# Kernel optimization log

Hardware: AMD Instinct MI355X
Metric: run time of the kernel (lower is better)

## Reference

```python
import jax, jax.numpy as jnp
import numpy as np

V = 32000   # vocab / input_size
H = 1024    # hidden_size (== embedding dim)
L = 2       # num_layers
B = 64      # batch
T = 256     # seq_len


def setup_inputs() -> dict:
    key = jax.random.key(0)
    ks = jax.random.split(key, 8)
    s = float(1.0 / np.sqrt(H))  # pytorch default uniform bound for LSTM/Linear
    return {
        "inputs": jax.random.randint(ks[0], (B, T), 0, V),
        "embed_table": jax.random.normal(ks[1], (V, H), jnp.float32),
        "W_ih": jax.random.uniform(ks[2], (L, 4 * H, H), jnp.float32, -s, s),
        "W_hh": jax.random.uniform(ks[3], (L, 4 * H, H), jnp.float32, -s, s),
        "b_ih": jax.random.uniform(ks[4], (L, 4 * H), jnp.float32, -s, s),
        "b_hh": jax.random.uniform(ks[5], (L, 4 * H), jnp.float32, -s, s),
        "W_proj": jax.random.uniform(ks[6], (V, H), jnp.float32, -s, s),
        "b_proj": jnp.zeros((V,), jnp.float32),  # module fills bias with 0
    }


def _lstm_layer(x, Wih, Whh, bih, bhh):
    # x: [B, T, H]. Precompute input contribution for all steps (one big GEMM).
    xg = jnp.einsum("bth,gh->btg", x, Wih) + bih + bhh  # [B, T, 4H]
    h0 = jnp.zeros((x.shape[0], Whh.shape[1]), x.dtype)
    c0 = h0

    def step(carry, xt):
        h, c = carry
        gates = xt + h @ Whh.T  # [B, 4H]
        i, f, g, o = jnp.split(gates, 4, axis=-1)  # pytorch gate order i,f,g,o
        i = jax.nn.sigmoid(i)
        f = jax.nn.sigmoid(f)
        g = jnp.tanh(g)
        o = jax.nn.sigmoid(o)
        c = f * c + i * g
        h = o * jnp.tanh(c)
        return (h, c), h

    (hT, cT), ys = jax.lax.scan(step, (h0, c0), jnp.swapaxes(xg, 0, 1))
    return jnp.swapaxes(ys, 0, 1), hT, cT  # [B,T,H], [B,H], [B,H]


def reference(inputs, embed_table, W_ih, W_hh, b_ih, b_hh, W_proj, b_proj):
    x = embed_table[inputs]  # [B, T, H]
    h_n, c_n = [], []
    for l in range(L):  # small fixed layer loop
        x, hT, cT = _lstm_layer(x, W_ih[l], W_hh[l], b_ih[l], b_hh[l])
        h_n.append(hT)
        c_n.append(cT)
    last_output = x[:, -1]                      # squeeze(output[:, -1]) with B>1 -> [B, H]
    logits = last_output @ W_proj.T + b_proj    # [B, V]
    return last_output, logits, jnp.stack(h_n), jnp.stack(c_n)
```

## Files before the change

kernel.cpp:

```cpp
#include <hip/hip_runtime.h>
#include <hip/hip_bf16.h>
#include <stdint.h>
#include <stddef.h>

typedef __hip_bfloat16 bf16;
typedef __attribute__((ext_vector_type(8))) short bfrag;
typedef __attribute__((ext_vector_type(4))) float ffrag;

#define HDIM 1024
#define BATCH 64
#define TSTEPS 256
#define GDIM 4096
#define VOCAB 32000

#define HSLOT 16384ull

__device__ __forceinline__ float b2f(bf16 x) { return __bfloat162float(x); }
__device__ __forceinline__ bf16 f2b(float x) { return __float2bfloat16(x); }
__device__ __forceinline__ short f2bs(float x) {
  bf16 b = __float2bfloat16(x);
  return *reinterpret_cast<short*>(&b);
}
__device__ __forceinline__ float bs2f(unsigned short u) {
  union { unsigned int i; float f; } v;
  v.i = ((unsigned int)u) << 16;
  return v.f;
}
__device__ __forceinline__ ffrag mfma16(bfrag a, bfrag b, ffrag c) {
  return __builtin_amdgcn_mfma_f32_16x16x32_bf16(a, b, c, 0, 0, 0);
}
__device__ __forceinline__ float sigm(float x) { return 1.0f / (1.0f + __expf(-x)); }
__device__ __forceinline__ float tanhfast(float x) {
  float e = __expf(2.0f * x);
  return 1.0f - 2.0f / (e + 1.0f);
}

__device__ __forceinline__ void store_u16_agent(unsigned short* p, unsigned short v) {
  __hip_atomic_store(p, v, __ATOMIC_RELAXED, __HIP_MEMORY_SCOPE_AGENT);
}
__device__ __forceinline__ unsigned long long load_u64_agent(const unsigned long long* p) {
  return __hip_atomic_load(p, __ATOMIC_RELAXED, __HIP_MEMORY_SCOPE_AGENT);
}
__device__ __forceinline__ void store_u32_agent(unsigned* p, unsigned v) {
  __hip_atomic_store(p, v, __ATOMIC_RELAXED, __HIP_MEMORY_SCOPE_AGENT);
}

__global__ void convert_bf16_kernel(const float* __restrict__ src, bf16* __restrict__ dst, int n4) {
  int i = blockIdx.x * 256 + threadIdx.x;
  if (i >= n4) return;
  float4 v = reinterpret_cast<const float4*>(src)[i];
  ushort4 o;
  o.x = (unsigned short)f2bs(v.x);
  o.y = (unsigned short)f2bs(v.y);
  o.z = (unsigned short)f2bs(v.z);
  o.w = (unsigned short)f2bs(v.w);
  reinterpret_cast<ushort4*>(dst)[i] = o;
}

__global__ void embed_kernel(const int* __restrict__ ids, const float* __restrict__ table,
                             bf16* __restrict__ x, int n4) {
  int i = blockIdx.x * 256 + threadIdx.x;
  if (i >= n4) return;
  int row = i >> 8;
  int c4 = i & 255;
  int tok = ids[row];
  float4 v = reinterpret_cast<const float4*>(table)[(size_t)tok * 256 + c4];
  ushort4 o;
  o.x = (unsigned short)f2bs(v.x);
  o.y = (unsigned short)f2bs(v.y);
  o.z = (unsigned short)f2bs(v.z);
  o.w = (unsigned short)f2bs(v.w);
  reinterpret_cast<ushort4*>(x)[i] = o;
}

#define BMX 128
#define BNX 128
#define BKX 64

template<int LYR>
__launch_bounds__(256, 2)
__global__ void gemm_xg_kernel(const bf16* __restrict__ A,
                               const bf16* __restrict__ W,
                               const float* __restrict__ bih,
                               const float* __restrict__ bhh,
                               bf16* __restrict__ xg) {
  __shared__ bf16 As[BMX][BKX + 8];
  __shared__ bf16 Bs[BNX][BKX + 8];
  const int n0 = blockIdx.x * BNX;
  const int m0 = blockIdx.y * BMX;
  const int tid = threadIdx.x;
  const int w = tid >> 6, l = tid & 63;
  const int wm = (w >> 1) * 64, wn = (w & 1) * 64;
  const int lr = l & 15, lk = (l >> 4) * 8;

  ffrag acc[4][4];
#pragma unroll
  for (int i = 0; i < 4; ++i)
#pragma unroll
    for (int j = 0; j < 4; ++j) acc[i][j] = ffrag{0.f, 0.f, 0.f, 0.f};

  const int sr = tid >> 1, sh = (tid & 1) * 32;
  for (int kb = 0; kb < HDIM; kb += BKX) {
    __syncthreads();
    {
      if (LYR == 0) {
        const uint4* ga = reinterpret_cast<const uint4*>(&A[(size_t)(m0 + sr) * HDIM + kb + sh]);
        uint4* la = reinterpret_cast<uint4*>(&As[sr][sh]);
        la[0] = ga[0]; la[1] = ga[1]; la[2] = ga[2]; la[3] = ga[3];
      } else {
        const unsigned long long* hb = (const unsigned long long*)A;
        const int m = m0 + sr;
        const size_t tb = (size_t)(255 - (m >> 6)) * HSLOT + (m & 63);
        const int kg0 = (kb + sh) >> 3;
#pragma unroll
        for (int ii = 0; ii < 4; ++ii) {
          unsigned long long lo = hb[tb + (size_t)(kg0 + ii) * 64];
          unsigned long long hi = hb[tb + 8192 + (size_t)(kg0 + ii) * 64];
          *(unsigned long long*)&As[sr][sh + ii * 8]     = lo;
          *(unsigned long long*)&As[sr][sh + ii * 8 + 4] = hi;
        }
      }
      const uint4* gb = reinterpret_cast<const uint4*>(&W[(size_t)(n0 + sr) * HDIM + kb + sh]);
      uint4* lb = reinterpret_cast<uint4*>(&Bs[sr][sh]);
      lb[0] = gb[0]; lb[1] = gb[1]; lb[2] = gb[2]; lb[3] = gb[3];
    }
    __syncthreads();
#pragma unroll
    for (int ks = 0; ks < 2; ++ks) {
      const int ko = ks * 32 + lk;
      bfrag af[4], bfv[4];
#pragma unroll
      for (int i = 0; i < 4; ++i)
        af[i] = *reinterpret_cast<const bfrag*>(&As[wm + i * 16 + lr][ko]);
#pragma unroll
      for (int j = 0; j < 4; ++j)
        bfv[j] = *reinterpret_cast<const bfrag*>(&Bs[wn + j * 16 + lr][ko]);
#pragma unroll
      for (int i = 0; i < 4; ++i)
#pragma unroll
        for (int j = 0; j < 4; ++j)
          acc[i][j] = mfma16(af[i], bfv[j], acc[i][j]);
    }
  }
  const int rg = (l >> 4) * 4;
#pragma unroll
  for (int j = 0; j < 4; ++j) {
    const int n = n0 + wn + j * 16 + lr;
    const float bias = bih[n] + bhh[n];
    const int q = n >> 10, g = (n & 1023) >> 3, jj = n & 7;
    bf16* base = xg + (size_t)(q * 128 + g) * 16384 * 8 + jj;
#pragma unroll
    for (int i = 0; i < 4; ++i) {
#pragma unroll
      for (int r = 0; r < 4; ++r) {
        const int m = m0 + wm + i * 16 + rg + r;
        base[(size_t)m * 8] = f2b(acc[i][j][r] + bias);
      }
    }
  }
}

__launch_bounds__(128, 1)
__global__ void lstm_seq_kernel(const bf16* __restrict__ xg,
                                const bf16* __restrict__ Whh,
                                bf16* hist,
                                float* __restrict__ out_h,
                                float* __restrict__ out_c,
                                float* __restrict__ out_last,
                                unsigned* __restrict__ flags,
                                int xbs, int xts) {
  __shared__ float gxp[2][16][33];
  const int wgid = blockIdx.x;
  const int bg = wgid & 3, cg = wgid >> 2;
  const int tid = threadIdx.x;
  const int w = tid >> 6, l = tid & 63;
  const int lr = l & 15, lkg = l >> 4;
  const int kh = w, kbase = kh * 512;

  bfrag breg0[16], breg1[16];
  {
    const int q = lr >> 2, ja = lr & 3;
    const size_t g0 = ((size_t)q * HDIM + cg * 8 + ja) * HDIM + kbase + lkg * 8;
    const size_t g1 = ((size_t)q * HDIM + cg * 8 + 4 + ja) * HDIM + kbase + lkg * 8;
#pragma unroll
    for (int ks = 0; ks < 16; ++ks) {
      breg0[ks] = *reinterpret_cast<const bfrag*>(&Whh[g0 + ks * 32]);
      breg1[ks] = *reinterpret_cast<const bfrag*>(&Whh[g1 + ks * 32]);
    }
  }

  const int eb = tid & 15;
  const int ejj = tid >> 4;
  const int b_glob = bg * 16 + eb;
  const int j_glob = cg * 8 + ejj;
  const int set = ejj >> 2, jn = ejj & 3;
  float c = 0.0f;

  unsigned long long* hb = (unsigned long long*)hist;
  const size_t hbase = (size_t)(kh * 64 + lkg) * 64 + bg * 16 + lr;

  const bf16* xq0 = xg + (size_t)(0 * 128 + cg) * 16384 * 8 + ejj;
  const bf16* xq1 = xg + (size_t)(1 * 128 + cg) * 16384 * 8 + ejj;
  const bf16* xq2 = xg + (size_t)(2 * 128 + cg) * 16384 * 8 + ejj;
  const bf16* xq3 = xg + (size_t)(3 * 128 + cg) * 16384 * 8 + ejj;
  unsigned short xv0, xv1, xv2, xv3;
  {
    const size_t xidx = (size_t)b_glob * xbs;
    xv0 = *(const unsigned short*)&xq0[xidx * 8];
    xv1 = *(const unsigned short*)&xq1[xidx * 8];
    xv2 = *(const unsigned short*)&xq2[xidx * 8];
    xv3 = *(const unsigned short*)&xq3[xidx * 8];
  }

  const unsigned long long* fv = (const unsigned long long*)flags + (size_t)bg * 128;

#pragma unroll 1
  for (int t = 0; t < TSTEPS; ++t) {
    if (t > 0) {
      const unsigned tt = (unsigned)t;
      for (;;) {
        unsigned long long fa = load_u64_agent(&fv[l]);
        unsigned long long fb = load_u64_agent(&fv[64 + l]);
        int ok = ((unsigned)fa >= tt) && ((unsigned)(fa >> 32) >= tt) &&
                 ((unsigned)fb >= tt) && ((unsigned)(fb >> 32) >= tt);
        if (__all(ok)) break;
        __builtin_amdgcn_s_sleep(1);
      }
    }
    __builtin_amdgcn_sched_barrier(0);
    asm volatile("" ::: "memory");

    const unsigned long long* hin = hb + (size_t)(TSTEPS - t) * HSLOT;
    ffrag a0 = ffrag{0.f, 0.f, 0.f, 0.f};
    ffrag a1 = ffrag{0.f, 0.f, 0.f, 0.f};
#pragma unroll
    for (int ks = 0; ks < 16; ++ks) {
      union { unsigned long long u[2]; bfrag f; } au;
      au.u[0] = hin[hbase + ks * 256];
      au.u[1] = hin[8192 + hbase + ks * 256];
      a0 = mfma16(au.f, breg0[ks], a0);
      a1 = mfma16(au.f, breg1[ks], a1);
    }
#pragma unroll
    for (int r = 0; r < 4; ++r) {
      gxp[kh][lkg * 4 + r][lr]      = a0[r];
      gxp[kh][lkg * 4 + r][16 + lr] = a1[r];
    }
    __syncthreads();

    const float gi = gxp[0][eb][set * 16 + jn]      + gxp[1][eb][set * 16 + jn]      + bs2f(xv0);
    const float gf = gxp[0][eb][set * 16 + 4 + jn]  + gxp[1][eb][set * 16 + 4 + jn]  + bs2f(xv1);
    const float gg = gxp[0][eb][set * 16 + 8 + jn]  + gxp[1][eb][set * 16 + 8 + jn]  + bs2f(xv2);
    const float go = gxp[0][eb][set * 16 + 12 + jn] + gxp[1][eb][set * 16 + 12 + jn] + bs2f(xv3);
    const float iv = sigm(gi), fvv = sigm(gf), gv = tanhfast(gg), ov = sigm(go);
    c = fvv * c + iv * gv;
    const float h = ov * tanhfast(c);
    const unsigned short hbits = (unsigned short)f2bs(h);

    unsigned long long* hout = hb + (size_t)(255 - t) * HSLOT;
    unsigned short* hp = (unsigned short*)(hout + (size_t)set * 8192 + cg * 64 + b_glob) + jn;
    store_u16_agent(hp, hbits);

    if (t < TSTEPS - 1) {
      __builtin_amdgcn_s_waitcnt(0);
      if (l == 0) store_u32_agent(&flags[bg * 256 + cg * 2 + w], (unsigned)(t + 1));
      const size_t xidx = (size_t)b_glob * xbs + (size_t)(t + 1) * xts;
      xv0 = *(const unsigned short*)&xq0[xidx * 8];
      xv1 = *(const unsigned short*)&xq1[xidx * 8];
      xv2 = *(const unsigned short*)&xq2[xidx * 8];
      xv3 = *(const unsigned short*)&xq3[xidx * 8];
    } else {
      out_h[(size_t)b_glob * HDIM + j_glob] = h;
      out_c[(size_t)b_glob * HDIM + j_glob] = c;
      if (out_last) out_last[(size_t)b_glob * HDIM + j_glob] = h;
    }
  }
}

__launch_bounds__(256, 2)
__global__ void logits_kernel(const bf16* __restrict__ hfin,
                              const float* __restrict__ Wp,
                              const float* __restrict__ bp,
                              float* __restrict__ out) {
  const int tid = threadIdx.x;
  const int w = tid >> 6, l = tid & 63;
  const int lr = l & 15, lkg = l >> 4, lk = lkg * 8;
  const int col = blockIdx.x * 64 + w * 16 + lr;
  const float* wrow = &Wp[(size_t)col * HDIM];
  const unsigned long long* hb = (const unsigned long long*)hfin;
  ffrag acc[4];
#pragma unroll
  for (int i = 0; i < 4; ++i) acc[i] = ffrag{0.f, 0.f, 0.f, 0.f};
#pragma unroll 2
  for (int ks = 0; ks < 32; ++ks) {
    const int k = ks * 32 + lk;
    float4 wa = *reinterpret_cast<const float4*>(&wrow[k]);
    float4 wb = *reinterpret_cast<const float4*>(&wrow[k + 4]);
    bfrag bv;
    bv[0] = f2bs(wa.x); bv[1] = f2bs(wa.y); bv[2] = f2bs(wa.z); bv[3] = f2bs(wa.w);
    bv[4] = f2bs(wb.x); bv[5] = f2bs(wb.y); bv[6] = f2bs(wb.z); bv[7] = f2bs(wb.w);
    const size_t kg = (size_t)(ks * 4 + lkg);
#pragma unroll
    for (int i = 0; i < 4; ++i) {
      union { unsigned long long u[2]; bfrag f; } av;
      av.u[0] = hb[kg * 64 + i * 16 + lr];
      av.u[1] = hb[8192 + kg * 64 + i * 16 + lr];
      acc[i] = mfma16(av.f, bv, acc[i]);
    }
  }
  const float bias = bp[col];
#pragma unroll
  for (int i = 0; i < 4; ++i) {
#pragma unroll
    for (int r = 0; r < 4; ++r) {
      const int b = i * 16 + (l >> 4) * 4 + r;
      out[(size_t)b * VOCAB + col] = acc[i][r] + bias;
    }
  }
}

extern "C" void kernel_launch(void* const* d_in, const int* in_sizes, int n_in,
                              void* d_out, int out_size, void* d_ws, size_t ws_size,
                              hipStream_t stream) {
  const int*   ids   = (const int*)d_in[0];
  const float* table = (const float*)d_in[1];
  const float* Wih   = (const float*)d_in[2];
  const float* Whh   = (const float*)d_in[3];
  const float* bih   = (const float*)d_in[4];
  const float* bhh   = (const float*)d_in[5];
  const float* Wp    = (const float*)d_in[6];
  const float* bp    = (const float*)d_in[7];
  float* out = (float*)d_out;

  char* ws = (char*)d_ws;
  const size_t HISTB = 257ull * 131072ull;
  const size_t OFF_XG  = 0;
  const size_t OFF_HA  = OFF_XG + (size_t)512 * 16384 * 8 * 2;
  const size_t OFF_HB  = OFF_HA + HISTB;
  const size_t OFF_WIH = OFF_HB + HISTB;
  const size_t OFF_WHH = OFF_WIH + (size_t)2 * GDIM * HDIM * 2;
  const size_t OFF_SYNC= OFF_WHH + (size_t)2 * GDIM * HDIM * 2;

  bf16* xg    = (bf16*)(ws + OFF_XG);
  bf16* xb    = (bf16*)(ws + OFF_HA);
  bf16* histA = (bf16*)(ws + OFF_HA);
  bf16* histB = (bf16*)(ws + OFF_HB);
  bf16* wihb  = (bf16*)(ws + OFF_WIH);
  bf16* whhb  = (bf16*)(ws + OFF_WHH);
  unsigned* sync = (unsigned*)(ws + OFF_SYNC);

  (void)hipMemsetAsync(sync, 0, 16384, stream);
  (void)hipMemsetAsync(ws + OFF_HA + 33554432ull, 0, 131072, stream);
  (void)hipMemsetAsync(ws + OFF_HB + 33554432ull, 0, 131072, stream);

  const int nconv4 = 2 * GDIM * HDIM / 4;
  convert_bf16_kernel<<<nconv4 / 256, 256, 0, stream>>>(Wih, wihb, nconv4);
  convert_bf16_kernel<<<nconv4 / 256, 256, 0, stream>>>(Whh, whhb, nconv4);
  const int nemb4 = BATCH * TSTEPS * HDIM / 4;
  embed_kernel<<<nemb4 / 256, 256, 0, stream>>>(ids, table, xb, nemb4);

  float* out_last   = out;
  float* out_logits = out + 65536;
  float* out_hn     = out + 2113536;
  float* out_cn     = out + 2244608;

  gemm_xg_kernel<0><<<dim3(GDIM / BNX, (BATCH * TSTEPS) / BMX), 256, 0, stream>>>(
      xb, wihb, bih, bhh, xg);
  lstm_seq_kernel<<<512, 128, 0, stream>>>(
      xg, whhb, histA, out_hn, out_cn, nullptr, sync, 256, 1);

  gemm_xg_kernel<1><<<dim3(GDIM / BNX, (BATCH * TSTEPS) / BMX), 256, 0, stream>>>(
      histA, wihb + (size_t)GDIM * HDIM, bih + GDIM, bhh + GDIM, xg);
  lstm_seq_kernel<<<512, 128, 0, stream>>>(
      xg, whhb + (size_t)GDIM * HDIM, histB,
      out_hn + (size_t)BATCH * HDIM, out_cn + (size_t)BATCH * HDIM,
      out_last, sync + 1024, 1, 64);

  logits_kernel<<<VOCAB / 64, 256, 0, stream>>>(histB, Wp, bp, out_logits);
}
```

Before: 2.315 ms.

## Fuse both LSTM layers into one wavefront-pipelined persistent kernel

The separate layer-2 input GEMM and the two sequential recurrence kernels are replaced by one persistent kernel with 768 blocks. 256 blocks run the layer-1 recurrence, and 512 blocks run layer 2, computing the W_ih·y and W_hh·h contributions per step from register-resident weights. Layer 2 step s waits on layer-1 flags for step s, so the two layers overlap as a wavefront. This removes a full GEMM pass and one kernel's serial latency. The cost is more per-step MFMA work in the layer-2 blocks and a requirement that all 768 blocks be co-resident (3 per CU), or the spin-waits can deadlock.

```diff
diff --git a/kernel.cpp b/kernel.cpp
--- a/kernel.cpp
+++ b/kernel.cpp
@@ -6,6 +6,7 @@
 typedef __hip_bfloat16 bf16;
 typedef __attribute__((ext_vector_type(8))) short bfrag;
 typedef __attribute__((ext_vector_type(4))) float ffrag;
+typedef unsigned long long u64;
 
 #define HDIM 1024
 #define BATCH 64
@@ -15,7 +16,6 @@
 
 #define HSLOT 16384ull
 
-__device__ __forceinline__ float b2f(bf16 x) { return __bfloat162float(x); }
 __device__ __forceinline__ bf16 f2b(float x) { return __float2bfloat16(x); }
 __device__ __forceinline__ short f2bs(float x) {
   bf16 b = __float2bfloat16(x);
@@ -38,7 +38,7 @@
 __device__ __forceinline__ void store_u16_agent(unsigned short* p, unsigned short v) {
   __hip_atomic_store(p, v, __ATOMIC_RELAXED, __HIP_MEMORY_SCOPE_AGENT);
 }
-__device__ __forceinline__ unsigned long long load_u64_agent(const unsigned long long* p) {
+__device__ __forceinline__ u64 load_u64_agent(const u64* p) {
   return __hip_atomic_load(p, __ATOMIC_RELAXED, __HIP_MEMORY_SCOPE_AGENT);
 }
 __device__ __forceinline__ void store_u32_agent(unsigned* p, unsigned v) {
@@ -77,7 +77,6 @@
 #define BNX 128
 #define BKX 64
 
-template<int LYR>
 __launch_bounds__(256, 2)
 __global__ void gemm_xg_kernel(const bf16* __restrict__ A,
                                const bf16* __restrict__ W,
@@ -103,23 +102,9 @@
   for (int kb = 0; kb < HDIM; kb += BKX) {
     __syncthreads();
     {
-      if (LYR == 0) {
-        const uint4* ga = reinterpret_cast<const uint4*>(&A[(size_t)(m0 + sr) * HDIM + kb + sh]);
-        uint4* la = reinterpret_cast<uint4*>(&As[sr][sh]);
-        la[0] = ga[0]; la[1] = ga[1]; la[2] = ga[2]; la[3] = ga[3];
-      } else {
-        const unsigned long long* hb = (const unsigned long long*)A;
-        const int m = m0 + sr;
-        const size_t tb = (size_t)(255 - (m >> 6)) * HSLOT + (m & 63);
-        const int kg0 = (kb + sh) >> 3;
-#pragma unroll
-        for (int ii = 0; ii < 4; ++ii) {
-          unsigned long long lo = hb[tb + (size_t)(kg0 + ii) * 64];
-          unsigned long long hi = hb[tb + 8192 + (size_t)(kg0 + ii) * 64];
-          *(unsigned long long*)&As[sr][sh + ii * 8]     = lo;
-          *(unsigned long long*)&As[sr][sh + ii * 8 + 4] = hi;
-        }
-      }
+      const uint4* ga = reinterpret_cast<const uint4*>(&A[(size_t)(m0 + sr) * HDIM + kb + sh]);
+      uint4* la = reinterpret_cast<uint4*>(&As[sr][sh]);
+      la[0] = ga[0]; la[1] = ga[1]; la[2] = ga[2]; la[3] = ga[3];
       const uint4* gb = reinterpret_cast<const uint4*>(&W[(size_t)(n0 + sr) * HDIM + kb + sh]);
       uint4* lb = reinterpret_cast<uint4*>(&Bs[sr][sh]);
       lb[0] = gb[0]; lb[1] = gb[1]; lb[2] = gb[2]; lb[3] = gb[3];
@@ -160,119 +145,221 @@
   }
 }
 
-__launch_bounds__(128, 1)
-__global__ void lstm_seq_kernel(const bf16* __restrict__ xg,
-                                const bf16* __restrict__ Whh,
-                                bf16* hist,
-                                float* __restrict__ out_h,
-                                float* __restrict__ out_c,
-                                float* __restrict__ out_last,
-                                unsigned* __restrict__ flags,
-                                int xbs, int xts) {
-  __shared__ float gxp[2][16][33];
-  const int wgid = blockIdx.x;
-  const int bg = wgid & 3, cg = wgid >> 2;
+__launch_bounds__(256, 3)
+__global__ void fused2_kernel(const bf16* __restrict__ xg,
+                              const bf16* __restrict__ whh1,
+                              const bf16* __restrict__ whh2,
+                              const bf16* __restrict__ wih2,
+                              const float* __restrict__ bih2,
+                              const float* __restrict__ bhh2,
+                              bf16* histA, bf16* histB,
+                              float* __restrict__ out_h1, float* __restrict__ out_c1,
+                              float* __restrict__ out_h2, float* __restrict__ out_c2,
+                              float* __restrict__ out_last,
+                              unsigned* __restrict__ fL1,
+                              unsigned* __restrict__ fL2) {
+  __shared__ float gxp[2][16][65];
+  const int id = blockIdx.x;
   const int tid = threadIdx.x;
   const int w = tid >> 6, l = tid & 63;
   const int lr = l & 15, lkg = l >> 4;
-  const int kh = w, kbase = kh * 512;
-
-  bfrag breg0[16], breg1[16];
-  {
-    const int q = lr >> 2, ja = lr & 3;
-    const size_t g0 = ((size_t)q * HDIM + cg * 8 + ja) * HDIM + kbase + lkg * 8;
-    const size_t g1 = ((size_t)q * HDIM + cg * 8 + 4 + ja) * HDIM + kbase + lkg * 8;
-#pragma unroll
-    for (int ks = 0; ks < 16; ++ks) {
-      breg0[ks] = *reinterpret_cast<const bfrag*>(&Whh[g0 + ks * 32]);
-      breg1[ks] = *reinterpret_cast<const bfrag*>(&Whh[g1 + ks * 32]);
-    }
-  }
-
-  const int eb = tid & 15;
-  const int ejj = tid >> 4;
-  const int b_glob = bg * 16 + eb;
-  const int j_glob = cg * 8 + ejj;
-  const int set = ejj >> 2, jn = ejj & 3;
-  float c = 0.0f;
-
-  unsigned long long* hb = (unsigned long long*)hist;
-  const size_t hbase = (size_t)(kh * 64 + lkg) * 64 + bg * 16 + lr;
-
-  const bf16* xq0 = xg + (size_t)(0 * 128 + cg) * 16384 * 8 + ejj;
-  const bf16* xq1 = xg + (size_t)(1 * 128 + cg) * 16384 * 8 + ejj;
-  const bf16* xq2 = xg + (size_t)(2 * 128 + cg) * 16384 * 8 + ejj;
-  const bf16* xq3 = xg + (size_t)(3 * 128 + cg) * 16384 * 8 + ejj;
-  unsigned short xv0, xv1, xv2, xv3;
-  {
-    const size_t xidx = (size_t)b_glob * xbs;
-    xv0 = *(const unsigned short*)&xq0[xidx * 8];
-    xv1 = *(const unsigned short*)&xq1[xidx * 8];
-    xv2 = *(const unsigned short*)&xq2[xidx * 8];
-    xv3 = *(const unsigned short*)&xq3[xidx * 8];
-  }
-
-  const unsigned long long* fv = (const unsigned long long*)flags + (size_t)bg * 128;
+  const int kh = w >> 1;
+  const int q = lr >> 2, jn = lr & 3;
+
+  if (id < 256) {
+    const int bg = id & 3, cg16 = id >> 2;
+    const int ch = w & 1;
+    bfrag breg0[16], breg1[16];
+    {
+      const int colbase = cg16 * 16 + ch * 8;
+      const size_t r0 = ((size_t)q * HDIM + colbase + jn) * HDIM + kh * 512 + lkg * 8;
+      const size_t r1 = ((size_t)q * HDIM + colbase + 4 + jn) * HDIM + kh * 512 + lkg * 8;
+#pragma unroll
+      for (int ks = 0; ks < 16; ++ks) {
+        breg0[ks] = *reinterpret_cast<const bfrag*>(&whh1[r0 + ks * 32]);
+        breg1[ks] = *reinterpret_cast<const bfrag*>(&whh1[r1 + ks * 32]);
+      }
+    }
+    const int eb = tid & 15, cl = tid >> 4;
+    const int gpl = cg16 * 2 + (cl >> 3);
+    const int xjj = cl & 7;
+    const int kgs = cg16 * 2 + (cl >> 3);
+    const int shalf = (cl >> 2) & 1, sjj = cl & 3;
+    float c = 0.0f;
+
+    u64* hb = (u64*)histA;
+    const size_t arow = (size_t)(kh * 64 + lkg) * 64 + bg * 16 + lr;
+    const u64* fv = (const u64*)fL1 + (size_t)bg * 128;
+    const unsigned short* xgu = (const unsigned short*)xg;
+
+    unsigned short xn[4];
+#pragma unroll
+    for (int qq = 0; qq < 4; ++qq)
+      xn[qq] = xgu[(((size_t)qq * 128 + gpl) * 16384 + (size_t)(bg * 16 + eb) * 256) * 8 + xjj];
 
 #pragma unroll 1
-  for (int t = 0; t < TSTEPS; ++t) {
-    if (t > 0) {
-      const unsigned tt = (unsigned)t;
-      for (;;) {
-        unsigned long long fa = load_u64_agent(&fv[l]);
-        unsigned long long fb = load_u64_agent(&fv[64 + l]);
-        int ok = ((unsigned)fa >= tt) && ((unsigned)(fa >> 32) >= tt) &&
-                 ((unsigned)fb >= tt) && ((unsigned)(fb >> 32) >= tt);
-        if (__all(ok)) break;
-        __builtin_amdgcn_s_sleep(1);
-      }
-    }
-    __builtin_amdgcn_sched_barrier(0);
-    asm volatile("" ::: "memory");
-
-    const unsigned long long* hin = hb + (size_t)(TSTEPS - t) * HSLOT;
-    ffrag a0 = ffrag{0.f, 0.f, 0.f, 0.f};
-    ffrag a1 = ffrag{0.f, 0.f, 0.f, 0.f};
-#pragma unroll
-    for (int ks = 0; ks < 16; ++ks) {
-      union { unsigned long long u[2]; bfrag f; } au;
-      au.u[0] = hin[hbase + ks * 256];
-      au.u[1] = hin[8192 + hbase + ks * 256];
-      a0 = mfma16(au.f, breg0[ks], a0);
-      a1 = mfma16(au.f, breg1[ks], a1);
-    }
-#pragma unroll
-    for (int r = 0; r < 4; ++r) {
-      gxp[kh][lkg * 4 + r][lr]      = a0[r];
-      gxp[kh][lkg * 4 + r][16 + lr] = a1[r];
-    }
-    __syncthreads();
-
-    const float gi = gxp[0][eb][set * 16 + jn]      + gxp[1][eb][set * 16 + jn]      + bs2f(xv0);
-    const float gf = gxp[0][eb][set * 16 + 4 + jn]  + gxp[1][eb][set * 16 + 4 + jn]  + bs2f(xv1);
-    const float gg = gxp[0][eb][set * 16 + 8 + jn]  + gxp[1][eb][set * 16 + 8 + jn]  + bs2f(xv2);
-    const float go = gxp[0][eb][set * 16 + 12 + jn] + gxp[1][eb][set * 16 + 12 + jn] + bs2f(xv3);
-    const float iv = sigm(gi), fvv = sigm(gf), gv = tanhfast(gg), ov = sigm(go);
-    c = fvv * c + iv * gv;
-    const float h = ov * tanhfast(c);
-    const unsigned short hbits = (unsigned short)f2bs(h);
-
-    unsigned long long* hout = hb + (size_t)(255 - t) * HSLOT;
-    unsigned short* hp = (unsigned short*)(hout + (size_t)set * 8192 + cg * 64 + b_glob) + jn;
-    store_u16_agent(hp, hbits);
-
-    if (t < TSTEPS - 1) {
+    for (int t = 0; t < TSTEPS; ++t) {
+      if (t > 0) {
+        const unsigned tt = (unsigned)t;
+        for (;;) {
+          u64 fa = load_u64_agent(&fv[l]);
+          u64 fb = load_u64_agent(&fv[64 + l]);
+          int ok = ((unsigned)fa >= tt) && ((unsigned)(fa >> 32) >= tt) &&
+                   ((unsigned)fb >= tt) && ((unsigned)(fb >> 32) >= tt);
+          if (__all(ok)) break;
+          __builtin_amdgcn_s_sleep(1);
+        }
+      }
+      __builtin_amdgcn_sched_barrier(0);
+      asm volatile("" ::: "memory");
+
+      const u64* hin = hb + (size_t)(TSTEPS - t) * HSLOT;
+      ffrag a0 = ffrag{0.f, 0.f, 0.f, 0.f};
+      ffrag a1 = ffrag{0.f, 0.f, 0.f, 0.f};
+#pragma unroll
+      for (int ks = 0; ks < 16; ++ks) {
+        union { u64 u[2]; bfrag f; } au;
+        au.u[0] = hin[arow + ks * 256];
+        au.u[1] = hin[8192 + arow + ks * 256];
+        a0 = mfma16(au.f, breg0[ks], a0);
+        a1 = mfma16(au.f, breg1[ks], a1);
+      }
+      {
+        const int cb = (w & 1) * 8;
+#pragma unroll
+        for (int r = 0; r < 4; ++r) {
+          gxp[kh][lkg * 4 + r][q * 16 + cb + jn]     = a0[r];
+          gxp[kh][lkg * 4 + r][q * 16 + cb + 4 + jn] = a1[r];
+        }
+      }
+      __syncthreads();
+
+      const float gi = gxp[0][eb][cl]      + gxp[1][eb][cl]      + bs2f(xn[0]);
+      const float gf = gxp[0][eb][16 + cl] + gxp[1][eb][16 + cl] + bs2f(xn[1]);
+      const float gg = gxp[0][eb][32 + cl] + gxp[1][eb][32 + cl] + bs2f(xn[2]);
+      const float go = gxp[0][eb][48 + cl] + gxp[1][eb][48 + cl] + bs2f(xn[3]);
+      c = sigm(gf) * c + sigm(gi) * tanhfast(gg);
+      const float h = sigm(go) * tanhfast(c);
+
+      u64* hout = hb + (size_t)(255 - t) * HSLOT;
+      store_u16_agent((unsigned short*)(hout + (size_t)shalf * 8192 + kgs * 64 + bg * 16 + eb) + sjj,
+                      (unsigned short)f2bs(h));
+      if (t == TSTEPS - 1) {
+        const int col = cg16 * 16 + cl;
+        out_h1[(size_t)(bg * 16 + eb) * HDIM + col] = h;
+        out_c1[(size_t)(bg * 16 + eb) * HDIM + col] = c;
+      }
       __builtin_amdgcn_s_waitcnt(0);
-      if (l == 0) store_u32_agent(&flags[bg * 256 + cg * 2 + w], (unsigned)(t + 1));
-      const size_t xidx = (size_t)b_glob * xbs + (size_t)(t + 1) * xts;
-      xv0 = *(const unsigned short*)&xq0[xidx * 8];
-      xv1 = *(const unsigned short*)&xq1[xidx * 8];
-      xv2 = *(const unsigned short*)&xq2[xidx * 8];
-      xv3 = *(const unsigned short*)&xq3[xidx * 8];
-    } else {
-      out_h[(size_t)b_glob * HDIM + j_glob] = h;
-      out_c[(size_t)b_glob * HDIM + j_glob] = c;
-      if (out_last) out_last[(size_t)b_glob * HDIM + j_glob] = h;
+      if (l == 0) store_u32_agent(&fL1[bg * 256 + cg16 * 4 + w], (unsigned)(t + 1));
+      if (t < TSTEPS - 1) {
+#pragma unroll
+        for (int qq = 0; qq < 4; ++qq)
+          xn[qq] = xgu[(((size_t)qq * 128 + gpl) * 16384 +
+                        (size_t)(bg * 16 + eb) * 256 + t + 1) * 8 + xjj];
+      }
+      __syncthreads();
+      __builtin_amdgcn_sched_barrier(0);
+    }
+  } else {
+    const int sid = id - 256;
+    const int bg = sid & 3, cg8 = sid >> 2;
+    const int ch4 = w & 1;
+    bfrag wregH[16], wregY[16];
+    {
+      const int colbase = cg8 * 8 + ch4 * 4;
+      const size_t rr = ((size_t)q * HDIM + colbase + jn) * HDIM + kh * 512 + lkg * 8;
+#pragma unroll
+      for (int ks = 0; ks < 16; ++ks) {
+        wregH[ks] = *reinterpret_cast<const bfrag*>(&whh2[rr + ks * 32]);
+        wregY[ks] = *reinterpret_cast<const bfrag*>(&wih2[rr + ks * 32]);
+      }
+    }
+    const int eb = tid & 15, jc = tid >> 4;
+    float biasq[4];
+    if (tid < 128) {
+#pragma unroll
+      for (int qq = 0; qq < 4; ++qq) {
+        const int n = qq * HDIM + cg8 * 8 + jc;
+        biasq[qq] = bih2[n] + bhh2[n];
+      }
+    }
+    float c = 0.0f;
+
+    const u64* hbA = (const u64*)histA;
+    u64* hbB = (u64*)histB;
+    const size_t arow = (size_t)(kh * 64 + lkg) * 64 + bg * 16 + lr;
+    const u64* f1 = (const u64*)fL1 + (size_t)bg * 128;
+    const u64* f2d = (const u64*)fL2 + (size_t)bg * 64;
+
+#pragma unroll 1
+    for (int s = 0; s < TSTEPS; ++s) {
+      {
+        const unsigned tt = (unsigned)(s + 1);
+        for (;;) {
+          u64 fa = load_u64_agent(&f1[l]);
+          u64 fb = load_u64_agent(&f1[64 + l]);
+          int ok = ((unsigned)fa >= tt) && ((unsigned)(fa >> 32) >= tt) &&
+                   ((unsigned)fb >= tt) && ((unsigned)(fb >> 32) >= tt);
+          if (__all(ok)) break;
+          __builtin_amdgcn_s_sleep(2);
+        }
+      }
+      if (s > 0) {
+        const unsigned tt = (unsigned)s;
+        for (;;) {
+          u64 v = load_u64_agent(&f2d[l]);
+          int ok = ((unsigned)v >= tt) && ((unsigned)(v >> 32) >= tt);
+          if (__all(ok)) break;
+          __builtin_amdgcn_s_sleep(1);
+        }
+      }
+      __builtin_amdgcn_sched_barrier(0);
+      asm volatile("" ::: "memory");
+
+      const u64* yin = hbA + (size_t)(255 - s) * HSLOT;
+      const u64* hin = hbB + (size_t)(256 - s) * HSLOT;
+      ffrag acc = ffrag{0.f, 0.f, 0.f, 0.f};
+#pragma unroll
+      for (int ks = 0; ks < 16; ++ks) {
+        union { u64 u[2]; bfrag f; } au;
+        au.u[0] = yin[arow + ks * 256];
+        au.u[1] = yin[8192 + arow + ks * 256];
+        acc = mfma16(au.f, wregY[ks], acc);
+      }
+#pragma unroll
+      for (int ks = 0; ks < 16; ++ks) {
+        union { u64 u[2]; bfrag f; } au;
+        au.u[0] = hin[arow + ks * 256];
+        au.u[1] = hin[8192 + arow + ks * 256];
+        acc = mfma16(au.f, wregH[ks], acc);
+      }
+#pragma unroll
+      for (int r = 0; r < 4; ++r)
+        gxp[kh][lkg * 4 + r][q * 8 + ch4 * 4 + jn] = acc[r];
+      __syncthreads();
+
+      if (tid < 128) {
+        const float gi = gxp[0][eb][jc]      + gxp[1][eb][jc]      + biasq[0];
+        const float gf = gxp[0][eb][8 + jc]  + gxp[1][eb][8 + jc]  + biasq[1];
+        const float gg = gxp[0][eb][16 + jc] + gxp[1][eb][16 + jc] + biasq[2];
+        const float go = gxp[0][eb][24 + jc] + gxp[1][eb][24 + jc] + biasq[3];
+        c = sigm(gf) * c + sigm(gi) * tanhfast(gg);
+        const float h = sigm(go) * tanhfast(c);
+        u64* hout = hbB + (size_t)(255 - s) * HSLOT;
+        store_u16_agent((unsigned short*)(hout + (size_t)(jc >> 2) * 8192 + cg8 * 64 + bg * 16 + eb) +
+                            (jc & 3),
+                        (unsigned short)f2bs(h));
+        if (s == TSTEPS - 1) {
+          const int col = cg8 * 8 + jc;
+          out_h2[(size_t)(bg * 16 + eb) * HDIM + col] = h;
+          out_c2[(size_t)(bg * 16 + eb) * HDIM + col] = c;
+          out_last[(size_t)(bg * 16 + eb) * HDIM + col] = h;
+        }
+        __builtin_amdgcn_s_waitcnt(0);
+      }
+      __syncthreads();
+      if (tid == 0) store_u32_agent(&fL2[bg * 128 + cg8], (unsigned)(s + 1));
+      __builtin_amdgcn_sched_barrier(0);
     }
   }
 }
@@ -287,7 +374,7 @@
   const int lr = l & 15, lkg = l >> 4, lk = lkg * 8;
   const int col = blockIdx.x * 64 + w * 16 + lr;
   const float* wrow = &Wp[(size_t)col * HDIM];
-  const unsigned long long* hb = (const unsigned long long*)hfin;
+  const u64* hb = (const u64*)hfin;
   ffrag acc[4];
 #pragma unroll
   for (int i = 0; i < 4; ++i) acc[i] = ffrag{0.f, 0.f, 0.f, 0.f};
@@ -302,7 +389,7 @@
     const size_t kg = (size_t)(ks * 4 + lkg);
 #pragma unroll
     for (int i = 0; i < 4; ++i) {
-      union { unsigned long long u[2]; bfrag f; } av;
+      union { u64 u[2]; bfrag f; } av;
       av.u[0] = hb[kg * 64 + i * 16 + lr];
       av.u[1] = hb[8192 + kg * 64 + i * 16 + lr];
       acc[i] = mfma16(av.f, bv, acc[i]);
@@ -333,11 +420,11 @@
   float* out = (float*)d_out;
 
   char* ws = (char*)d_ws;
-  const size_t HISTB = 257ull * 131072ull;
+  const size_t HISTB_SZ = 257ull * 131072ull;
   const size_t OFF_XG  = 0;
   const size_t OFF_HA  = OFF_XG + (size_t)512 * 16384 * 8 * 2;
-  const size_t OFF_HB  = OFF_HA + HISTB;
-  const size_t OFF_WIH = OFF_HB + HISTB;
+  const size_t OFF_HB  = OFF_HA + HISTB_SZ;
+  const size_t OFF_WIH = OFF_HB + HISTB_SZ;
   const size_t OFF_WHH = OFF_WIH + (size_t)2 * GDIM * HDIM * 2;
   const size_t OFF_SYNC= OFF_WHH + (size_t)2 * GDIM * HDIM * 2;
 
@@ -348,6 +435,8 @@
   bf16* wihb  = (bf16*)(ws + OFF_WIH);
   bf16* whhb  = (bf16*)(ws + OFF_WHH);
   unsigned* sync = (unsigned*)(ws + OFF_SYNC);
+  unsigned* fL1 = sync;
+  unsigned* fL2 = sync + 1024;
 
   (void)hipMemsetAsync(sync, 0, 16384, stream);
   (void)hipMemsetAsync(ws + OFF_HA + 33554432ull, 0, 131072, stream);
@@ -364,17 +453,14 @@
   float* out_hn     = out + 2113536;
   float* out_cn     = out + 2244608;
 
-  gemm_xg_kernel<0><<<dim3(GDIM / BNX, (BATCH * TSTEPS) / BMX), 256, 0, stream>>>(
+  gemm_xg_kernel<<<dim3(GDIM / BNX, (BATCH * TSTEPS) / BMX), 256, 0, stream>>>(
       xb, wihb, bih, bhh, xg);
-  lstm_seq_kernel<<<512, 128, 0, stream>>>(
-      xg, whhb, histA, out_hn, out_cn, nullptr, sync, 256, 1);
-
-  gemm_xg_kernel<1><<<dim3(GDIM / BNX, (BATCH * TSTEPS) / BMX), 256, 0, stream>>>(
-      histA, wihb + (size_t)GDIM * HDIM, bih + GDIM, bhh + GDIM, xg);
-  lstm_seq_kernel<<<512, 128, 0, stream>>>(
-      xg, whhb + (size_t)GDIM * HDIM, histB,
-      out_hn + (size_t)BATCH * HDIM, out_cn + (size_t)BATCH * HDIM,
-      out_last, sync + 1024, 1, 64);
+
+  fused2_kernel<<<768, 256, 0, stream>>>(
+      xg, whhb, whhb + (size_t)GDIM * HDIM, wihb + (size_t)GDIM * HDIM,
+      bih + GDIM, bhh + GDIM, histA, histB,
+      out_hn, out_cn, out_hn + BATCH * HDIM, out_cn + BATCH * HDIM, out_last,
+      fL1, fL2);
 
   logits_kernel<<<VOCAB / 64, 256, 0, stream>>>(histB, Wp, bp, out_logits);
 }
```

New measurement: 3.339 ms. +44.2%, slower.

## Halve LSTM recurrence workgroups with 256-thread blocks and one flag per block

Applied to the files above, without the earlier changes.

The persistent LSTM recurrence kernel now runs 256 workgroups of 256 threads, each handling 16 hidden columns with four waves (two K-halves by two column halves), where before it ran 512 workgroups of 128 threads handling 8 columns each. Each workgroup now publishes a single step flag after a block barrier, instead of one flag per wave. Waiters therefore poll 64 u32 flags per batch group rather than 256. The aim is to cut grid-wide synchronisation traffic and the number of participants in each step's handshake. The cost is an extra __syncthreads per step and possibly worse spreading of work across CUs.

```diff
diff --git a/kernel.cpp b/kernel.cpp
--- a/kernel.cpp
+++ b/kernel.cpp
@@ -6,6 +6,7 @@
 typedef __hip_bfloat16 bf16;
 typedef __attribute__((ext_vector_type(8))) short bfrag;
 typedef __attribute__((ext_vector_type(4))) float ffrag;
+typedef unsigned long long u64;
 
 #define HDIM 1024
 #define BATCH 64
@@ -15,7 +16,6 @@
 
 #define HSLOT 16384ull
 
-__device__ __forceinline__ float b2f(bf16 x) { return __bfloat162float(x); }
 __device__ __forceinline__ bf16 f2b(float x) { return __float2bfloat16(x); }
 __device__ __forceinline__ short f2bs(float x) {
   bf16 b = __float2bfloat16(x);
@@ -38,7 +38,7 @@
 __device__ __forceinline__ void store_u16_agent(unsigned short* p, unsigned short v) {
   __hip_atomic_store(p, v, __ATOMIC_RELAXED, __HIP_MEMORY_SCOPE_AGENT);
 }
-__device__ __forceinline__ unsigned long long load_u64_agent(const unsigned long long* p) {
+__device__ __forceinline__ unsigned load_u32_agent(const unsigned* p) {
   return __hip_atomic_load(p, __ATOMIC_RELAXED, __HIP_MEMORY_SCOPE_AGENT);
 }
 __device__ __forceinline__ void store_u32_agent(unsigned* p, unsigned v) {
@@ -108,16 +108,16 @@
         uint4* la = reinterpret_cast<uint4*>(&As[sr][sh]);
         la[0] = ga[0]; la[1] = ga[1]; la[2] = ga[2]; la[3] = ga[3];
       } else {
-        const unsigned long long* hb = (const unsigned long long*)A;
+        const u64* hb = (const u64*)A;
         const int m = m0 + sr;
         const size_t tb = (size_t)(255 - (m >> 6)) * HSLOT + (m & 63);
         const int kg0 = (kb + sh) >> 3;
 #pragma unroll
         for (int ii = 0; ii < 4; ++ii) {
-          unsigned long long lo = hb[tb + (size_t)(kg0 + ii) * 64];
-          unsigned long long hi = hb[tb + 8192 + (size_t)(kg0 + ii) * 64];
-          *(unsigned long long*)&As[sr][sh + ii * 8]     = lo;
-          *(unsigned long long*)&As[sr][sh + ii * 8 + 4] = hi;
+          u64 lo = hb[tb + (size_t)(kg0 + ii) * 64];
+          u64 hi = hb[tb + 8192 + (size_t)(kg0 + ii) * 64];
+          *(u64*)&As[sr][sh + ii * 8]     = lo;
+          *(u64*)&As[sr][sh + ii * 8 + 4] = hi;
         }
       }
       const uint4* gb = reinterpret_cast<const uint4*>(&W[(size_t)(n0 + sr) * HDIM + kb + sh]);
@@ -160,7 +160,7 @@
   }
 }
 
-__launch_bounds__(128, 1)
+__launch_bounds__(256, 1)
 __global__ void lstm_seq_kernel(const bf16* __restrict__ xg,
                                 const bf16* __restrict__ Whh,
                                 bf16* hist,
@@ -169,111 +169,104 @@
                                 float* __restrict__ out_last,
                                 unsigned* __restrict__ flags,
                                 int xbs, int xts) {
-  __shared__ float gxp[2][16][33];
-  const int wgid = blockIdx.x;
-  const int bg = wgid & 3, cg = wgid >> 2;
+  __shared__ float gxp[2][16][65];
+  const int id = blockIdx.x;
+  const int bg = id & 3, cg16 = id >> 2;
   const int tid = threadIdx.x;
   const int w = tid >> 6, l = tid & 63;
   const int lr = l & 15, lkg = l >> 4;
-  const int kh = w, kbase = kh * 512;
+  const int kh = w >> 1, ch = w & 1;
+  const int q = lr >> 2, jn = lr & 3;
 
   bfrag breg0[16], breg1[16];
   {
-    const int q = lr >> 2, ja = lr & 3;
-    const size_t g0 = ((size_t)q * HDIM + cg * 8 + ja) * HDIM + kbase + lkg * 8;
-    const size_t g1 = ((size_t)q * HDIM + cg * 8 + 4 + ja) * HDIM + kbase + lkg * 8;
+    const int colbase = cg16 * 16 + ch * 8;
+    const size_t r0 = ((size_t)q * HDIM + colbase + jn) * HDIM + kh * 512 + lkg * 8;
+    const size_t r1 = ((size_t)q * HDIM + colbase + 4 + jn) * HDIM + kh * 512 + lkg * 8;
 #pragma unroll
     for (int ks = 0; ks < 16; ++ks) {
-      breg0[ks] = *reinterpret_cast<const bfrag*>(&Whh[g0 + ks * 32]);
-      breg1[ks] = *reinterpret_cast<const bfrag*>(&Whh[g1 + ks * 32]);
-    }
-  }
-
-  const int eb = tid & 15;
-  const int ejj = tid >> 4;
+      breg0[ks] = *reinterpret_cast<const bfrag*>(&Whh[r0 + ks * 32]);
+      breg1[ks] = *reinterpret_cast<const bfrag*>(&Whh[r1 + ks * 32]);
+    }
+  }
+
+  const int eb = tid & 15, cl = tid >> 4;
   const int b_glob = bg * 16 + eb;
-  const int j_glob = cg * 8 + ejj;
-  const int set = ejj >> 2, jn = ejj & 3;
+  const int gpl = cg16 * 2 + (cl >> 3);
+  const int xjj = cl & 7;
+  const int shalf = (cl >> 2) & 1, sjj = cl & 3;
   float c = 0.0f;
 
-  unsigned long long* hb = (unsigned long long*)hist;
-  const size_t hbase = (size_t)(kh * 64 + lkg) * 64 + bg * 16 + lr;
-
-  const bf16* xq0 = xg + (size_t)(0 * 128 + cg) * 16384 * 8 + ejj;
-  const bf16* xq1 = xg + (size_t)(1 * 128 + cg) * 16384 * 8 + ejj;
-  const bf16* xq2 = xg + (size_t)(2 * 128 + cg) * 16384 * 8 + ejj;
-  const bf16* xq3 = xg + (size_t)(3 * 128 + cg) * 16384 * 8 + ejj;
-  unsigned short xv0, xv1, xv2, xv3;
-  {
-    const size_t xidx = (size_t)b_glob * xbs;
-    xv0 = *(const unsigned short*)&xq0[xidx * 8];
-    xv1 = *(const unsigned short*)&xq1[xidx * 8];
-    xv2 = *(const unsigned short*)&xq2[xidx * 8];
-    xv3 = *(const unsigned short*)&xq3[xidx * 8];
-  }
-
-  const unsigned long long* fv = (const unsigned long long*)flags + (size_t)bg * 128;
+  u64* hb = (u64*)hist;
+  const size_t arow = (size_t)(kh * 64 + lkg) * 64 + bg * 16 + lr;
+  const unsigned* fv = flags + bg * 64;
+  const unsigned short* xgu = (const unsigned short*)xg;
+
+  unsigned short xn[4];
+#pragma unroll
+  for (int qq = 0; qq < 4; ++qq)
+    xn[qq] = xgu[(((size_t)qq * 128 + gpl) * 16384 + (size_t)b_glob * xbs) * 8 + xjj];
 
 #pragma unroll 1
   for (int t = 0; t < TSTEPS; ++t) {
     if (t > 0) {
       const unsigned tt = (unsigned)t;
       for (;;) {
-        unsigned long long fa = load_u64_agent(&fv[l]);
-        unsigned long long fb = load_u64_agent(&fv[64 + l]);
-        int ok = ((unsigned)fa >= tt) && ((unsigned)(fa >> 32) >= tt) &&
-                 ((unsigned)fb >= tt) && ((unsigned)(fb >> 32) >= tt);
-        if (__all(ok)) break;
+        unsigned f = load_u32_agent(&fv[l]);
+        if (__all((int)(f >= tt))) break;
         __builtin_amdgcn_s_sleep(1);
       }
     }
     __builtin_amdgcn_sched_barrier(0);
     asm volatile("" ::: "memory");
 
-    const unsigned long long* hin = hb + (size_t)(TSTEPS - t) * HSLOT;
+    const u64* hin = hb + (size_t)(TSTEPS - t) * HSLOT;
     ffrag a0 = ffrag{0.f, 0.f, 0.f, 0.f};
     ffrag a1 = ffrag{0.f, 0.f, 0.f, 0.f};
 #pragma unroll
     for (int ks = 0; ks < 16; ++ks) {
-      union { unsigned long long u[2]; bfrag f; } au;
-      au.u[0] = hin[hbase + ks * 256];
-      au.u[1] = hin[8192 + hbase + ks * 256];
+      union { u64 u[2]; bfrag f; } au;
+      au.u[0] = hin[arow + ks * 256];
+      au.u[1] = hin[8192 + arow + ks * 256];
       a0 = mfma16(au.f, breg0[ks], a0);
       a1 = mfma16(au.f, breg1[ks], a1);
     }
-#pragma unroll
-    for (int r = 0; r < 4; ++r) {
-      gxp[kh][lkg * 4 + r][lr]      = a0[r];
-      gxp[kh][lkg * 4 + r][16 + lr] = a1[r];
+    {
+      const int cb = ch * 8;
+#pragma unroll
+      for (int r = 0; r < 4; ++r) {
+        gxp[kh][lkg * 4 + r][q * 16 + cb + jn]     = a0[r];
+        gxp[kh][lkg * 4 + r][q * 16 + cb + 4 + jn] = a1[r];
+      }
     }
     __syncthreads();
 
-    const float gi = gxp[0][eb][set * 16 + jn]      + gxp[1][eb][set * 16 + jn]      + bs2f(xv0);
-    const float gf = gxp[0][eb][set * 16 + 4 + jn]  + gxp[1][eb][set * 16 + 4 + jn]  + bs2f(xv1);
-    const float gg = gxp[0][eb][set * 16 + 8 + jn]  + gxp[1][eb][set * 16 + 8 + jn]  + bs2f(xv2);
-    const float go = gxp[0][eb][set * 16 + 12 + jn] + gxp[1][eb][set * 16 + 12 + jn] + bs2f(xv3);
-    const float iv = sigm(gi), fvv = sigm(gf), gv = tanhfast(gg), ov = sigm(go);
-    c = fvv * c + iv * gv;
-    const float h = ov * tanhfast(c);
-    const unsigned short hbits = (unsigned short)f2bs(h);
-
-    unsigned long long* hout = hb + (size_t)(255 - t) * HSLOT;
-    unsigned short* hp = (unsigned short*)(hout + (size_t)set * 8192 + cg * 64 + b_glob) + jn;
-    store_u16_agent(hp, hbits);
-
+    const float gi = gxp[0][eb][cl]      + gxp[1][eb][cl]      + bs2f(xn[0]);
+    const float gf = gxp[0][eb][16 + cl] + gxp[1][eb][16 + cl] + bs2f(xn[1]);
+    const float gg = gxp[0][eb][32 + cl] + gxp[1][eb][32 + cl] + bs2f(xn[2]);
+    const float go = gxp[0][eb][48 + cl] + gxp[1][eb][48 + cl] + bs2f(xn[3]);
+    c = sigm(gf) * c + sigm(gi) * tanhfast(gg);
+    const float h = sigm(go) * tanhfast(c);
+
+    u64* hout = hb + (size_t)(255 - t) * HSLOT;
+    store_u16_agent((unsigned short*)(hout + (size_t)shalf * 8192 + gpl * 64 + b_glob) + sjj,
+                    (unsigned short)f2bs(h));
+    if (t == TSTEPS - 1) {
+      const int col = cg16 * 16 + cl;
+      out_h[(size_t)b_glob * HDIM + col] = h;
+      out_c[(size_t)b_glob * HDIM + col] = c;
+      if (out_last) out_last[(size_t)b_glob * HDIM + col] = h;
+    }
+    __builtin_amdgcn_s_waitcnt(0);
+    __syncthreads();
     if (t < TSTEPS - 1) {
-      __builtin_amdgcn_s_waitcnt(0);
-      if (l == 0) store_u32_agent(&flags[bg * 256 + cg * 2 + w], (unsigned)(t + 1));
-      const size_t xidx = (size_t)b_glob * xbs + (size_t)(t + 1) * xts;
-      xv0 = *(const unsigned short*)&xq0[xidx * 8];
-      xv1 = *(const unsigned short*)&xq1[xidx * 8];
-      xv2 = *(const unsigned short*)&xq2[xidx * 8];
-      xv3 = *(const unsigned short*)&xq3[xidx * 8];
-    } else {
-      out_h[(size_t)b_glob * HDIM + j_glob] = h;
-      out_c[(size_t)b_glob * HDIM + j_glob] = c;
-      if (out_last) out_last[(size_t)b_glob * HDIM + j_glob] = h;
-    }
+      if (tid == 0) store_u32_agent(&flags[bg * 64 + cg16], (unsigned)(t + 1));
+#pragma unroll
+      for (int qq = 0; qq < 4; ++qq)
+        xn[qq] = xgu[(((size_t)qq * 128 + gpl) * 16384 +
+                      (size_t)b_glob * xbs + (size_t)(t + 1) * xts) * 8 + xjj];
+    }
+    __builtin_amdgcn_sched_barrier(0);
   }
 }
 
@@ -287,7 +280,7 @@
   const int lr = l & 15, lkg = l >> 4, lk = lkg * 8;
   const int col = blockIdx.x * 64 + w * 16 + lr;
   const float* wrow = &Wp[(size_t)col * HDIM];
-  const unsigned long long* hb = (const unsigned long long*)hfin;
+  const u64* hb = (const u64*)hfin;
   ffrag acc[4];
 #pragma unroll
   for (int i = 0; i < 4; ++i) acc[i] = ffrag{0.f, 0.f, 0.f, 0.f};
@@ -302,7 +295,7 @@
     const size_t kg = (size_t)(ks * 4 + lkg);
 #pragma unroll
     for (int i = 0; i < 4; ++i) {
-      union { unsigned long long u[2]; bfrag f; } av;
+      union { u64 u[2]; bfrag f; } av;
       av.u[0] = hb[kg * 64 + i * 16 + lr];
       av.u[1] = hb[8192 + kg * 64 + i * 16 + lr];
       acc[i] = mfma16(av.f, bv, acc[i]);
@@ -333,11 +326,11 @@
   float* out = (float*)d_out;
 
   char* ws = (char*)d_ws;
-  const size_t HISTB = 257ull * 131072ull;
+  const size_t HISTB_SZ = 257ull * 131072ull;
   const size_t OFF_XG  = 0;
   const size_t OFF_HA  = OFF_XG + (size_t)512 * 16384 * 8 * 2;
-  const size_t OFF_HB  = OFF_HA + HISTB;
-  const size_t OFF_WIH = OFF_HB + HISTB;
+  const size_t OFF_HB  = OFF_HA + HISTB_SZ;
+  const size_t OFF_WIH = OFF_HB + HISTB_SZ;
   const size_t OFF_WHH = OFF_WIH + (size_t)2 * GDIM * HDIM * 2;
   const size_t OFF_SYNC= OFF_WHH + (size_t)2 * GDIM * HDIM * 2;
 
@@ -366,15 +359,15 @@
 
   gemm_xg_kernel<0><<<dim3(GDIM / BNX, (BATCH * TSTEPS) / BMX), 256, 0, stream>>>(
       xb, wihb, bih, bhh, xg);
-  lstm_seq_kernel<<<512, 128, 0, stream>>>(
+  lstm_seq_kernel<<<256, 256, 0, stream>>>(
       xg, whhb, histA, out_hn, out_cn, nullptr, sync, 256, 1);
 
   gemm_xg_kernel<1><<<dim3(GDIM / BNX, (BATCH * TSTEPS) / BMX), 256, 0, stream>>>(
       histA, wihb + (size_t)GDIM * HDIM, bih + GDIM, bhh + GDIM, xg);
-  lstm_seq_kernel<<<512, 128, 0, stream>>>(
+  lstm_seq_kernel<<<256, 256, 0, stream>>>(
       xg, whhb + (size_t)GDIM * HDIM, histB,
       out_hn + (size_t)BATCH * HDIM, out_cn + (size_t)BATCH * HDIM,
-      out_last, sync + 1024, 1, 64);
+      out_last, sync + 256, 1, 64);
 
   logits_kernel<<<VOCAB / 64, 256, 0, stream>>>(histB, Wp, bp, out_logits);
 }
```

Measured after the change: 2.175 ms. -6.0%, faster.
